# Kernel optimization log

Measured on AMD Instinct MI355X. Metric: run time of the kernel, lower is better.

Reference implementation:

```python
import jax, jax.numpy as jnp
import numpy as np

S, N, F, E, H = 64, 1000, 64, 128, 2  # seq_len, nodes/graph, node_dim, emb_dim, heads
DEG = 8
C = E // H  # per-head channels


def setup_inputs() -> dict:
    key = jax.random.key(0)
    ks = jax.random.split(key, 16)
    Ntot = S * N
    Eg = N * DEG
    src = jax.random.randint(ks[0], (S, Eg), 0, N)
    dst = jax.random.randint(ks[1], (S, Eg), 0, N)
    off = (jnp.arange(S) * N)[:, None]
    edge_index = jnp.stack([(src + off).reshape(-1), (dst + off).reshape(-1)]).astype(jnp.int32)
    nfm = jax.random.normal(ks[2], (Ntot, F), jnp.float32)
    reachable = jax.random.uniform(ks[3], (S, N)) > 0.2
    reachable = reachable.at[:, 0].set(True)  # ensure each row has a reachable node
    h0 = jnp.zeros((N, E), jnp.float32)
    c0 = jnp.zeros((N, E), jnp.float32)

    def lin(k, i, o):
        return (jax.random.normal(k, (i, o), jnp.float32) / np.sqrt(i)).astype(jnp.float32)

    return dict(
        nfm=nfm, edge_index=edge_index, reachable=reachable, h0=h0, c0=c0,
        gat_W1=lin(ks[4], F, E), gat_b1=jnp.zeros((E,), jnp.float32),
        gat_att1=(jax.random.normal(ks[5], (H, C), jnp.float32) / np.sqrt(C)).astype(jnp.float32),
        gat_bias1=jnp.zeros((E,), jnp.float32),
        gat_W=(jax.random.normal(ks[6], (4, E, E), jnp.float32) / np.sqrt(E)).astype(jnp.float32),
        gat_b=jnp.zeros((4, E), jnp.float32),
        gat_att=(jax.random.normal(ks[7], (4, H, C), jnp.float32) / np.sqrt(C)).astype(jnp.float32),
        gat_bias=jnp.zeros((4, E), jnp.float32),
        lstm_Wih=(jax.random.normal(ks[8], (4 * E, E), jnp.float32) / np.sqrt(E)).astype(jnp.float32),
        lstm_Whh=(jax.random.normal(ks[9], (4 * E, E), jnp.float32) / np.sqrt(E)).astype(jnp.float32),
        lstm_bih=jnp.zeros((4 * E,), jnp.float32), lstm_bhh=jnp.zeros((4 * E,), jnp.float32),
        th6_W=lin(ks[10], E, E), th6_b=jnp.zeros((E,), jnp.float32),
        th7_W=lin(ks[11], E, E), th7_b=jnp.zeros((E,), jnp.float32),
        th5_W=lin(ks[12], 2 * E, 1), th5_b=jnp.zeros((1,), jnp.float32),
    )


def _gat_layer(x, src, dst, W, b, att, bias, Ntot):
    # GATv2Conv, share_weights=True: x_l == x_r = lin(x)
    Hh, Ch = att.shape
    xl = (x @ W + b).reshape(-1, Hh, Ch)                 # [Ntot,H,C]
    e = jax.nn.leaky_relu(xl[src] + xl[dst], 0.2)        # [Etot,H,C]
    logit = jnp.einsum('ehc,hc->eh', e, att)             # [Etot,H]
    m = jax.ops.segment_max(logit, dst, num_segments=Ntot)
    a = jnp.exp(logit - m[dst])                          # segment-stable softmax
    denom = jax.ops.segment_sum(a, dst, num_segments=Ntot)
    alpha = a / denom[dst]
    out = jax.ops.segment_sum(xl[src] * alpha[:, :, None], dst, num_segments=Ntot)
    return out.reshape(-1, Hh * Ch) + bias               # concat heads + bias


def _forward(nfm, edge_index, reachable, h0, c0, gat_W1, gat_b1, gat_att1, gat_bias1,
             gat_W, gat_b, gat_att, gat_bias, lstm_Wih, lstm_Whh, lstm_bih, lstm_bhh,
             th6_W, th6_b, th7_W, th7_b, th5_W, th5_b):
    Ntot = nfm.shape[0]
    loops = jnp.arange(Ntot, dtype=edge_index.dtype)     # add_self_loops=True
    src = jnp.concatenate([edge_index[0], loops])
    dst = jnp.concatenate([edge_index[1], loops])

    x = jax.nn.relu(_gat_layer(nfm, src, dst, gat_W1, gat_b1, gat_att1, gat_bias1, Ntot))
    for i in range(4):  # layers 2..5; no activation after last
        x = _gat_layer(x, src, dst, gat_W[i], gat_b[i], gat_att[i], gat_bias[i], Ntot)
        if i < 3:
            x = jax.nn.relu(x)

    mu = x.reshape(S, N, E)                              # [seq, batch(=nodes), emb]

    def step(carry, xt):
        h, c = carry
        g = xt @ lstm_Wih.T + lstm_bih + h @ lstm_Whh.T + lstm_bhh
        i_, f_, gg, o_ = jnp.split(g, 4, axis=-1)        # torch gate order i,f,g,o
        c = jax.nn.sigmoid(f_) * c + jax.nn.sigmoid(i_) * jnp.tanh(gg)
        h = jax.nn.sigmoid(o_) * jnp.tanh(c)
        return (h, c), h

    (hT, cT), mu = jax.lax.scan(step, (h0, c0), mu)      # mu: [S,N,E]

    meanpool = mu.mean(axis=1, keepdims=True)            # [S,1,E]
    gs = meanpool @ th6_W + th6_b
    la = mu @ th7_W + th7_b
    rep = jax.nn.relu(jnp.concatenate([jnp.broadcast_to(gs, la.shape), la], axis=-1))
    logits = (rep @ th5_W)[..., 0] + th5_b               # [S,N]
    logits = jnp.where(reachable, logits, -jnp.inf)
    prob = jax.nn.softmax(logits, axis=1)
    return prob, hT, cT


def reference(nfm, edge_index, reachable, h0, c0, gat_W1, gat_b1, gat_att1, gat_bias1,
              gat_W, gat_b, gat_att, gat_bias, lstm_Wih, lstm_Whh, lstm_bih, lstm_bhh,
              th6_W, th6_b, th7_W, th7_b, th5_W, th5_b):
    return _forward(nfm, edge_index, reachable, h0, c0, gat_W1, gat_b1, gat_att1, gat_bias1,
                    gat_W, gat_b, gat_att, gat_bias, lstm_Wih, lstm_Whh, lstm_bih, lstm_bhh,
                    th6_W, th6_b, th7_W, th7_b, th5_W, th5_b)
```

## Files before the change

kernel.cpp:

```cpp
#include <hip/hip_runtime.h>
#include <hip/hip_bf16.h>

#define SQ   64
#define NN   1000
#define NT   64000
#define EE   128
#define EG   512000
#define ET   576000

#define WS_XA      0ull
#define WS_XB      33000000ull
#define WS_ROWPTR  66000000ull
#define WS_CURSOR  66300000ull
#define WS_SRCS    66600000ull
#define WS_INCL    69000000ull
#define WS_BSUM    69300000ull
#define WS_BOFF    69302048ull
#define WS_MODE    69304096ull
#define WS_WQA     70000000ull
#define WS_WQB     70262144ull
#define WS_AS      70600000ull
#define WS_LOGIT2  70700000ull
#define WS2_XC     33000000ull
#define WS2_BFRAG  164100000ull
#define WS2_GHI    164300000ull
#define WS2_GLO    164650000ull
#define WS2_B512   165000000ull
#define WS2_MODE   165010000ull
#define WS2_AS     165020000ull
#define WS2_LOGIT2 165100000ull
#define WS2_NEED   165360000ull
#define G_W1    0
#define G_WL    8192
#define G_PROJ  73728
#define G_W7    139264

typedef __attribute__((ext_vector_type(8))) short short8;
typedef __attribute__((ext_vector_type(4))) float f32x4;

__device__ __forceinline__ float rdlane(float v, int l) {
    return __int_as_float(__builtin_amdgcn_readlane(__float_as_int(v), l));
}
__device__ __forceinline__ float sigm(float x) { return 1.0f / (1.0f + __expf(-x)); }
__device__ __forceinline__ float tanh_f(float x) {
    x = fminf(fmaxf(x, -30.0f), 30.0f);
    float e = __expf(2.0f * x);
    return (e - 1.0f) / (e + 1.0f);
}
__device__ __forceinline__ float tanh2(float x) {
    return 2.0f / (1.0f + __expf(-2.0f * x)) - 1.0f;
}
__device__ __forceinline__ ushort f2bf(float x) {
    unsigned u = __float_as_uint(x);
    unsigned r = (u + 0x7FFFu + ((u >> 16) & 1u)) >> 16;
    return (ushort)r;
}
__device__ __forceinline__ float bf2f(ushort h) {
    return __uint_as_float(((unsigned)h) << 16);
}

__global__ void detect_mode_k(const unsigned char* __restrict__ p, int* __restrict__ mode) {
    __shared__ int f0, f3;
    const int t = threadIdx.x;
    if (t == 0) { f0 = 0; f3 = 0; }
    __syncthreads();
    int l0 = 0, l3 = 0;
    for (int i = t; i < 16000; i += 256) {
        if (p[4 * i])     l0 = 1;
        if (p[4 * i + 3]) l3 = 1;
    }
    if (l0) atomicOr(&f0, 1);
    if (l3) atomicOr(&f3, 1);
    __syncthreads();
    if (t == 0) {
        int m;
        if (f0 && f3)      m = 1;
        else if (f0)       m = 0;
        else               m = 2;
        *mode = m;
    }
}

__global__ void zero_ints_k(int* __restrict__ p, int n) {
    int i = blockIdx.x * 256 + threadIdx.x;
    if (i < n) p[i] = 0;
}
__global__ void hist_k(const int* __restrict__ ei, int* __restrict__ deg) {
    int e = blockIdx.x * 256 + threadIdx.x;
    if (e < ET) {
        int d = (e < EG) ? ei[EG + e] : (e - EG);
        atomicAdd(deg + d, 1);
    }
}
__global__ void scan1_k(const int* __restrict__ deg, int* __restrict__ incl, int* __restrict__ bsum) {
    __shared__ int sh[256];
    const int t = threadIdx.x;
    const int i = blockIdx.x * 256 + t;
    sh[t] = deg[i];
    __syncthreads();
    for (int o = 1; o < 256; o <<= 1) {
        int add = (t >= o) ? sh[t - o] : 0;
        __syncthreads();
        sh[t] += add;
        __syncthreads();
    }
    incl[i] = sh[t];
    if (t == 255) bsum[blockIdx.x] = sh[255];
}
__global__ void scan2_k(const int* __restrict__ bsum, int* __restrict__ boff) {
    __shared__ int sh[256];
    const int t = threadIdx.x;
    int v = (t < 250) ? bsum[t] : 0;
    sh[t] = v;
    __syncthreads();
    for (int o = 1; o < 256; o <<= 1) {
        int add = (t >= o) ? sh[t - o] : 0;
        __syncthreads();
        sh[t] += add;
        __syncthreads();
    }
    if (t < 250) boff[t] = sh[t] - v;
}
__global__ void scan3_k(const int* __restrict__ incl, const int* __restrict__ boff,
                        int* __restrict__ rowptr, int* __restrict__ cursor_deg) {
    const int i = blockIdx.x * 256 + threadIdx.x;
    int total = incl[i] + boff[blockIdx.x];
    int excl  = total - cursor_deg[i];
    rowptr[i] = excl;
    cursor_deg[i] = excl;
    if (i == NT - 1) rowptr[NT] = total;
}
__global__ void fill_k(const int* __restrict__ ei, int* __restrict__ cursor, int* __restrict__ srcs) {
    int e = blockIdx.x * 256 + threadIdx.x;
    if (e < ET) {
        int s_, d_;
        if (e < EG) { s_ = ei[e]; d_ = ei[EG + e]; }
        else        { s_ = e - EG; d_ = s_; }
        int p = atomicAdd(cursor + d_, 1);
        srcs[p] = s_;
    }
}

__global__ void build_gfrag_k(const float* __restrict__ src, const int ks, const int ns,
                              const int K, ushort* __restrict__ dhi, ushort* __restrict__ dlo,
                              const int total) {
    int id = blockIdx.x * 256 + threadIdx.x;
    if (id < total) {
        int j = id & 7, lane = (id >> 3) & 63;
        int f = id >> 9;
        int KT = K >> 5;
        int nt = f / KT, kt = f - nt * KT;
        int n = nt * 16 + (lane & 15);
        int k = kt * 32 + ((lane >> 4) << 3) + j;
        float v = src[(size_t)k * ks + (size_t)n * ns];
        ushort h = f2bf(v);
        dhi[id] = h;
        dlo[id] = f2bf(v - bf2f(h));
    }
}
__global__ void bias512_k(const float* __restrict__ bih, const float* __restrict__ bhh,
                          float* __restrict__ b512) {
    int i = blockIdx.x * 256 + threadIdx.x;
    if (i < 512) b512[i] = bih[i] + bhh[i];
}

template <int KT>
__global__ __launch_bounds__(256) void gemm_mf(
    const float* __restrict__ x, const ushort* __restrict__ bhi,
    const ushort* __restrict__ blo, const float* __restrict__ bias,
    float* __restrict__ out, const int ldout)
{
    constexpr int K = KT * 32;
    __shared__ __align__(16) ushort ahi_s[64 * 136];
    __shared__ __align__(16) ushort alo_s[64 * 136];
    const int t = threadIdx.x;
    const int w = t >> 6, lane = t & 63;
    const int quad = lane >> 4, col = lane & 15;
    const int row0 = blockIdx.x * 64;
    const int col0 = blockIdx.y * 128;

    {
        const int r  = t >> 2;
        const int kc = (t & 3) * (K / 4);
        const float* xr = x + (size_t)(row0 + r) * K + kc;
        ushort* dh = ahi_s + r * 136 + kc;
        ushort* dl = alo_s + r * 136 + kc;
#pragma unroll
        for (int k = 0; k < K / 4; k += 4) {
            float4 v = *(const float4*)(xr + k);
            ushort h0_ = f2bf(v.x), h1_ = f2bf(v.y), h2_ = f2bf(v.z), h3_ = f2bf(v.w);
            ushort l0_ = f2bf(v.x - bf2f(h0_)), l1_ = f2bf(v.y - bf2f(h1_));
            ushort l2_ = f2bf(v.z - bf2f(h2_)), l3_ = f2bf(v.w - bf2f(h3_));
            *(uint2*)(dh + k) = make_uint2((uint)h0_ | ((uint)h1_ << 16),
                                           (uint)h2_ | ((uint)h3_ << 16));
            *(uint2*)(dl + k) = make_uint2((uint)l0_ | ((uint)l1_ << 16),
                                           (uint)l2_ | ((uint)l3_ << 16));
        }
    }
    __syncthreads();

    short8 ah[KT], al[KT];
#pragma unroll
    for (int kt = 0; kt < KT; kt++) {
        const int off = (w * 16 + col) * 136 + kt * 32 + quad * 8;
        ah[kt] = *(const short8*)(ahi_s + off);
        al[kt] = *(const short8*)(alo_s + off);
    }

    f32x4 acc[8];
#pragma unroll
    for (int q = 0; q < 8; q++) acc[q] = (f32x4){0.f, 0.f, 0.f, 0.f};

#pragma unroll
    for (int q = 0; q < 8; q++) {
#pragma unroll
        for (int kt = 0; kt < KT; kt++) {
            const int f = ((((col0 >> 4) + q) * KT + kt) * 64 + lane) * 8;
            short8 bh = *(const short8*)(bhi + f);
            short8 bl = *(const short8*)(blo + f);
            acc[q] = __builtin_amdgcn_mfma_f32_16x16x32_bf16(ah[kt], bh, acc[q], 0, 0, 0);
            acc[q] = __builtin_amdgcn_mfma_f32_16x16x32_bf16(al[kt], bh, acc[q], 0, 0, 0);
            acc[q] = __builtin_amdgcn_mfma_f32_16x16x32_bf16(ah[kt], bl, acc[q], 0, 0, 0);
        }
    }

#pragma unroll
    for (int q = 0; q < 8; q++) {
        float bv = bias[col0 + q * 16 + col];
#pragma unroll
        for (int r = 0; r < 4; r++) {
            out[(size_t)(row0 + w * 16 + quad * 4 + r) * ldout + col0 + q * 16 + col]
                = acc[q][r] + bv;
        }
    }
}

template <int K>
__global__ __launch_bounds__(256) void gemm3(
    const float* __restrict__ x, const float* __restrict__ W,
    const float* __restrict__ b, float* __restrict__ out)
{
    __shared__ float Wsh[64 * 128];
    __shared__ float xT[64][132];
    const int t = threadIdx.x;
    const int row0 = blockIdx.x * 128;
    const int cg = t & 15;
    const int rg = t >> 4;
    float4 acc[8][2];
#pragma unroll
    for (int r = 0; r < 8; r++) {
        acc[r][0] = make_float4(0.f, 0.f, 0.f, 0.f);
        acc[r][1] = make_float4(0.f, 0.f, 0.f, 0.f);
    }
    for (int k0 = 0; k0 < K; k0 += 64) {
        for (int i = t * 4; i < 64 * 128; i += 1024)
            *(float4*)(Wsh + i) = *(const float4*)(W + (size_t)k0 * 128 + i);
        for (int i = t * 4; i < 128 * 64; i += 1024) {
            int r = i >> 6, k = i & 63;
            float4 v = *(const float4*)(x + (size_t)(row0 + r) * K + k0 + k);
            xT[k + 0][r] = v.x; xT[k + 1][r] = v.y;
            xT[k + 2][r] = v.z; xT[k + 3][r] = v.w;
        }
        __syncthreads();
#pragma unroll 2
        for (int k = 0; k < 64; k++) {
            float4 w0 = *(const float4*)(Wsh + k * 128 + cg * 8);
            float4 w1 = *(const float4*)(Wsh + k * 128 + cg * 8 + 4);
            float4 x0 = *(const float4*)(&xT[k][rg * 8]);
            float4 x1 = *(const float4*)(&xT[k][rg * 8 + 4]);
            float xv[8] = {x0.x, x0.y, x0.z, x0.w, x1.x, x1.y, x1.z, x1.w};
#pragma unroll
            for (int r = 0; r < 8; r++) {
                acc[r][0].x += xv[r] * w0.x; acc[r][0].y += xv[r] * w0.y;
                acc[r][0].z += xv[r] * w0.z; acc[r][0].w += xv[r] * w0.w;
                acc[r][1].x += xv[r] * w1.x; acc[r][1].y += xv[r] * w1.y;
                acc[r][1].z += xv[r] * w1.z; acc[r][1].w += xv[r] * w1.w;
            }
        }
        __syncthreads();
    }
    float4 bv0 = *(const float4*)(b + cg * 8);
    float4 bv1 = *(const float4*)(b + cg * 8 + 4);
#pragma unroll
    for (int r = 0; r < 8; r++) {
        float4 o0, o1;
        o0.x = acc[r][0].x + bv0.x; o0.y = acc[r][0].y + bv0.y;
        o0.z = acc[r][0].z + bv0.z; o0.w = acc[r][0].w + bv0.w;
        o1.x = acc[r][1].x + bv1.x; o1.y = acc[r][1].y + bv1.y;
        o1.z = acc[r][1].z + bv1.z; o1.w = acc[r][1].w + bv1.w;
        float* op = out + (size_t)(row0 + rg * 8 + r) * 128 + cg * 8;
        *(float4*)(op) = o0;
        *(float4*)(op + 4) = o1;
    }
}

__global__ __launch_bounds__(256) void gat_fused_k(
    const float* __restrict__ xl, const int* __restrict__ rowptr,
    const int* __restrict__ srcs, const float* __restrict__ att,
    const float* __restrict__ bias, float* __restrict__ out, const int do_relu)
{
    const int lane = threadIdx.x & 63;
    const int b = blockIdx.x;
    const int g = b & 7;
    const int j = b >> 3;
    const int jq = j / 250;
    const int jj = j - jq * 250;
    const int s = g + 8 * jq;
    const int n = s * NN + jj * 4 + (threadIdx.x >> 6);

    const float2 a = *(const float2*)(att + lane * 2);
    const float2 xd = *(const float2*)(xl + (size_t)n * 128 + lane * 2);
    const int i0 = rowptr[n], i1 = rowptr[n + 1];

    float m0 = -1e30f, d0 = 0.f, ax0 = 0.f, ay0 = 0.f;
    float m1 = -1e30f, d1 = 0.f, ax1 = 0.f, ay1 = 0.f;

    int i = i0;
    int sv0 = srcs[i];
    int sv1 = (i + 1 < i1) ? srcs[i + 1] : 0;
    while (i + 1 < i1) {
        const float2 xs0 = *(const float2*)(xl + (size_t)sv0 * 128 + lane * 2);
        const float2 xs1 = *(const float2*)(xl + (size_t)sv1 * 128 + lane * 2);
        sv0 = (i + 2 < i1) ? srcs[i + 2] : 0;
        sv1 = (i + 3 < i1) ? srcs[i + 3] : 0;

        float u0 = xs0.x + xd.x, v0 = xs0.y + xd.y;
        float u1 = xs1.x + xd.x, v1 = xs1.y + xd.y;
        u0 = (u0 > 0.f) ? u0 : 0.2f * u0;  v0 = (v0 > 0.f) ? v0 : 0.2f * v0;
        u1 = (u1 > 0.f) ? u1 : 0.2f * u1;  v1 = (v1 > 0.f) ? v1 : 0.2f * v1;
        float p0 = u0 * a.x + v0 * a.y;
        float p1 = u1 * a.x + v1 * a.y;
        p0 += __shfl_xor(p0, 1, 32);   p1 += __shfl_xor(p1, 1, 32);
        p0 += __shfl_xor(p0, 2, 32);   p1 += __shfl_xor(p1, 2, 32);
        p0 += __shfl_xor(p0, 4, 32);   p1 += __shfl_xor(p1, 4, 32);
        p0 += __shfl_xor(p0, 8, 32);   p1 += __shfl_xor(p1, 8, 32);
        p0 += __shfl_xor(p0, 16, 32);  p1 += __shfl_xor(p1, 16, 32);

        float mn0 = fmaxf(m0, p0),  mn1 = fmaxf(m1, p1);
        float sc0 = __expf(m0 - mn0), sc1 = __expf(m1 - mn1);
        float w0 = __expf(p0 - mn0),  w1 = __expf(p1 - mn1);
        d0 = d0 * sc0 + w0;             d1 = d1 * sc1 + w1;
        ax0 = ax0 * sc0 + w0 * xs0.x;   ax1 = ax1 * sc1 + w1 * xs1.x;
        ay0 = ay0 * sc0 + w0 * xs0.y;   ay1 = ay1 * sc1 + w1 * xs1.y;
        m0 = mn0;                       m1 = mn1;
        i += 2;
    }
    if (i < i1) {
        const float2 xs0 = *(const float2*)(xl + (size_t)sv0 * 128 + lane * 2);
        float u0 = xs0.x + xd.x, v0 = xs0.y + xd.y;
        u0 = (u0 > 0.f) ? u0 : 0.2f * u0;  v0 = (v0 > 0.f) ? v0 : 0.2f * v0;
        float p0 = u0 * a.x + v0 * a.y;
        p0 += __shfl_xor(p0, 1, 32);
        p0 += __shfl_xor(p0, 2, 32);
        p0 += __shfl_xor(p0, 4, 32);
        p0 += __shfl_xor(p0, 8, 32);
        p0 += __shfl_xor(p0, 16, 32);
        float mn0 = fmaxf(m0, p0);
        float sc0 = __expf(m0 - mn0), w0 = __expf(p0 - mn0);
        d0 = d0 * sc0 + w0;
        ax0 = ax0 * sc0 + w0 * xs0.x;
        ay0 = ay0 * sc0 + w0 * xs0.y;
        m0 = mn0;
    }
    float mm = fmaxf(m0, m1);
    float s0 = __expf(m0 - mm), s1 = __expf(m1 - mm);
    float den = d0 * s0 + d1 * s1;
    float ax = ax0 * s0 + ax1 * s1;
    float ay = ay0 * s0 + ay1 * s1;

    float2 bv = *(const float2*)(bias + lane * 2);
    float inv = 1.f / den;
    float ox = ax * inv + bv.x, oy = ay * inv + bv.y;
    if (do_relu) { ox = fmaxf(ox, 0.f); oy = fmaxf(oy, 0.f); }
    *(float2*)(out + (size_t)n * 128 + lane * 2) = make_float2(ox, oy);
}

__global__ void build_wq_k(const float* __restrict__ Wih, const float* __restrict__ Whh,
                           float4* __restrict__ WQa, float4* __restrict__ WQb) {
    int id = blockIdx.x * 256 + threadIdx.x;
    if (id < 64 * 256) {
        int kp = id >> 8, t = id & 255;
        int j1 = t, j2 = t + 256;
        WQa[id] = make_float4(Wih[(size_t)j1 * 128 + 2 * kp], Whh[(size_t)j1 * 128 + 2 * kp],
                              Wih[(size_t)j1 * 128 + 2 * kp + 1], Whh[(size_t)j1 * 128 + 2 * kp + 1]);
        WQb[id] = make_float4(Wih[(size_t)j2 * 128 + 2 * kp], Whh[(size_t)j2 * 128 + 2 * kp],
                              Wih[(size_t)j2 * 128 + 2 * kp + 1], Whh[(size_t)j2 * 128 + 2 * kp + 1]);
    }
}

__global__ void build_bfrag_k(const float* __restrict__ Whh, ushort* __restrict__ Bfrag) {
    int id = blockIdx.x * 256 + threadIdx.x;
    if (id < 65536) {
        int j = id & 7, lane = (id >> 3) & 63, kt = (id >> 9) & 3, tile = id >> 11;
        int gate = tile * 16 + (lane & 15);
        int k = kt * 32 + ((lane >> 4) << 3) + j;
        Bfrag[id] = f2bf(Whh[(size_t)gate * 128 + k]);
    }
}

#define LSTM_GROUP(buf, gbase)                                                     \
    _Pragma("unroll")                                                              \
    for (int i_ = 0; i_ < 4; i_++) {                                               \
        const int kp_ = (gbase) * 4 + i_;                                          \
        const float4 qa_ = buf[i_];                                                \
        const float4 qb_ = buf[4 + i_];                                            \
        _Pragma("unroll")                                                          \
        for (int n_ = 0; n_ < 4; n_++) {                                           \
            const float sx0_ = rdlane(xr[n_].x, kp_);                              \
            const float sh0_ = rdlane(hr[n_].x, kp_);                              \
            const float sx1_ = rdlane(xr[n_].y, kp_);                              \
            const float sh1_ = rdlane(hr[n_].y, kp_);                              \
            acc1[n_] += sx0_ * qa_.x + sh0_ * qa_.y + sx1_ * qa_.z + sh1_ * qa_.w; \
            acc2[n_] += sx0_ * qb_.x + sh0_ * qb_.y + sx1_ * qb_.z + sh1_ * qb_.w; \
        }                                                                          \
    }

__global__ __launch_bounds__(256, 1) void lstm_k(
    float* __restrict__ mu, const float4* __restrict__ WQa, const float4* __restrict__ WQb,
    const float* __restrict__ bih, const float* __restrict__ bhh,
    const float* __restrict__ h0, const float* __restrict__ c0,
    float* __restrict__ hT, float* __restrict__ cT)
{
    const int t = threadIdx.x, lane = t & 63;
    const int n0 = blockIdx.x * 4;
    __shared__ float hsh[4][128];
    __shared__ float gsh[4][512];
    const float b1 = bih[t] + bhh[t];
    const float b2 = bih[t + 256] + bhh[t + 256];
    float creg[2];
#pragma unroll
    for (int q = 0; q < 2; q++) {
        int id = t + 256 * q;
        creg[q] = c0[(size_t)(n0 + (id >> 7)) * 128 + (id & 127)];
    }
    for (int i = t; i < 512; i += 256)
        hsh[i >> 7][i & 127] = h0[(size_t)(n0 + (i >> 7)) * 128 + (i & 127)];

    const float4* pA = WQa + t;
    const float4* pB = WQb + t;

    float2 xr[4], xnx[4];
#pragma unroll
    for (int n = 0; n < 4; n++)
        xr[n] = *(const float2*)(mu + (size_t)n0 * 128 + n * 128 + lane * 2);
    __syncthreads();

    for (int s = 0; s < SQ; s++) {
        float* xrow = mu + ((size_t)s * NN + n0) * 128;
        float2 hr[4];
#pragma unroll
        for (int n = 0; n < 4; n++) hr[n] = *(const float2*)(&hsh[n][lane * 2]);

        float4 bufA[8], bufB[8];
#pragma unroll
        for (int i = 0; i < 4; i++) { bufA[i] = pA[i * 256]; bufA[4 + i] = pB[i * 256]; }

        if (s + 1 < SQ) {
            const float* xrow2 = mu + ((size_t)(s + 1) * NN + n0) * 128;
#pragma unroll
            for (int n = 0; n < 4; n++) xnx[n] = *(const float2*)(xrow2 + n * 128 + lane * 2);
        }

        float acc1[4], acc2[4];
#pragma unroll
        for (int n = 0; n < 4; n++) { acc1[n] = b1; acc2[n] = b2; }

        for (int g = 0; g < 16; g += 2) {
#pragma unroll
            for (int i = 0; i < 4; i++) {
                bufB[i]     = pA[((g + 1) * 4 + i) * 256];
                bufB[4 + i] = pB[((g + 1) * 4 + i) * 256];
            }
            LSTM_GROUP(bufA, g)
            if (g < 14) {
#pragma unroll
                for (int i = 0; i < 4; i++) {
                    bufA[i]     = pA[((g + 2) * 4 + i) * 256];
                    bufA[4 + i] = pB[((g + 2) * 4 + i) * 256];
                }
            }
            LSTM_GROUP(bufB, g + 1)
        }

#pragma unroll
        for (int n = 0; n < 4; n++) { gsh[n][t] = acc1[n]; gsh[n][t + 256] = acc2[n]; }
        __syncthreads();
#pragma unroll
        for (int q = 0; q < 2; q++) {
            int id = t + 256 * q;
            int n = id >> 7, e = id & 127;
            float iv = gsh[n][e], fv = gsh[n][128 + e];
            float gv = gsh[n][256 + e], ov = gsh[n][384 + e];
            float c = sigm(fv) * creg[q] + sigm(iv) * tanh_f(gv);
            float h = sigm(ov) * tanh_f(c);
            creg[q] = c;
            hsh[n][e] = h;
            xrow[n * 128 + e] = h;
            if (s == SQ - 1) {
                hT[(size_t)(n0 + n) * 128 + e] = h;
                cT[(size_t)(n0 + n) * 128 + e] = c;
            }
        }
#pragma unroll
        for (int n = 0; n < 4; n++) xr[n] = xnx[n];
        __syncthreads();
    }
}

__global__ __launch_bounds__(512, 2) void lstm8_k(
    float* __restrict__ mu, const float* __restrict__ xC,
    const ushort* __restrict__ Bfrag,
    const float* __restrict__ h0, const float* __restrict__ c0,
    float* __restrict__ hT, float* __restrict__ cT)
{
    const int t = threadIdx.x;
    const int w = t >> 6, lane = t & 63;
    const int quad = lane >> 4, col = lane & 15;
    const int n0 = blockIdx.x * 4;
    const int enode = t >> 7;
    const int ech   = t & 127;

    __shared__ __align__(16) ushort hbuf[2][2][16 * 136];
    __shared__ float gsh[4][512];

    short8 bf[4][4];
#pragma unroll
    for (int g4 = 0; g4 < 4; g4++)
#pragma unroll
        for (int kt = 0; kt < 4; kt++) {
            int tile = g4 * 8 + w;
            bf[g4][kt] = *(const short8*)(Bfrag + (((tile * 4 + kt) * 64 + lane) << 3));
        }

    for (int i = t; i < 2048; i += 512) {
        int node = i >> 7, ee = i & 127;
        float v = (node < 4) ? h0[(size_t)(n0 + node) * 128 + ee] : 0.f;
        ushort hh = f2bf(v), hl = f2bf(v - bf2f(hh));
        hbuf[0][0][node * 136 + ee] = hh; hbuf[0][1][node * 136 + ee] = hl;
        hbuf[1][0][node * 136 + ee] = hh; hbuf[1][1][node * 136 + ee] = hl;
    }
    float cst = c0[(size_t)(n0 + enode) * 128 + ech];

    float xcr[4], xcn[4];
#pragma unroll
    for (int g4 = 0; g4 < 4; g4++)
        xcr[g4] = xC[((size_t)(n0 + enode)) * 512 + g4 * 128 + ech];
    __syncthreads();

    int p = 0;
    for (int s = 0; s < SQ; s++) {
        if (s + 1 < SQ) {
            const float* xn = xC + ((size_t)(s + 1) * NN + n0 + enode) * 512;
#pragma unroll
            for (int g4 = 0; g4 < 4; g4++)
                xcn[g4] = xn[g4 * 128 + ech];
        }

        short8 ahi[4], alo[4];
#pragma unroll
        for (int kt = 0; kt < 4; kt++) {
            ahi[kt] = *(const short8*)(&hbuf[p][0][col * 136 + kt * 32 + quad * 8]);
            alo[kt] = *(const short8*)(&hbuf[p][1][col * 136 + kt * 32 + quad * 8]);
        }

        f32x4 acc[4];
#pragma unroll
        for (int g4 = 0; g4 < 4; g4++) acc[g4] = (f32x4){0.f, 0.f, 0.f, 0.f};
#pragma unroll
        for (int kt = 0; kt < 4; kt++) {
#pragma unroll
            for (int g4 = 0; g4 < 4; g4++)
                acc[g4] = __builtin_amdgcn_mfma_f32_16x16x32_bf16(ahi[kt], bf[g4][kt], acc[g4], 0, 0, 0);
#pragma unroll
            for (int g4 = 0; g4 < 4; g4++)
                acc[g4] = __builtin_amdgcn_mfma_f32_16x16x32_bf16(alo[kt], bf[g4][kt], acc[g4], 0, 0, 0);
        }

        if (quad == 0) {
#pragma unroll
            for (int g4 = 0; g4 < 4; g4++)
#pragma unroll
                for (int r = 0; r < 4; r++)
                    gsh[r][(g4 * 8 + w) * 16 + col] = acc[g4][r];
        }
        __syncthreads();

        {
            float iv = gsh[enode][0 * 128 + ech] + xcr[0];
            float fv = gsh[enode][1 * 128 + ech] + xcr[1];
            float gv = gsh[enode][2 * 128 + ech] + xcr[2];
            float ov = gsh[enode][3 * 128 + ech] + xcr[3];
            float c = sigm(fv) * cst + sigm(iv) * tanh2(gv);
            float h = sigm(ov) * tanh2(c);
            cst = c;
            const int pn = p ^ 1;
            ushort hh = f2bf(h);
            hbuf[pn][0][enode * 136 + ech] = hh;
            hbuf[pn][1][enode * 136 + ech] = f2bf(h - bf2f(hh));
            mu[((size_t)s * NN + n0 + enode) * 128 + ech] = h;
            if (s == SQ - 1) {
                hT[(size_t)(n0 + enode) * 128 + ech] = h;
                cT[(size_t)(n0 + enode) * 128 + ech] = c;
            }
            p = pn;
        }
#pragma unroll
        for (int g4 = 0; g4 < 4; g4++) xcr[g4] = xcn[g4];
        __syncthreads();
    }
}

__global__ __launch_bounds__(256) void meanpool_gs_k(
    const float* __restrict__ mu, const float* __restrict__ W6,
    const float* __restrict__ b6, const float* __restrict__ w5,
    float* __restrict__ A)
{
    const int s = blockIdx.x, t = threadIdx.x;
    const int ch = t & 127, half = t >> 7;
    __shared__ float mp[128];
    __shared__ float red[256];
    float acc = 0.f;
    for (int n = half * 500; n < (half + 1) * 500; n++)
        acc += mu[((size_t)s * NN + n) * 128 + ch];
    red[t] = acc;
    __syncthreads();
    if (t < 128) mp[t] = (red[t] + red[t + 128]) * 0.001f;
    __syncthreads();
    float g = 0.f;
    if (t < 128) {
        g = b6[t];
        for (int k = 0; k < 128; k++) g += mp[k] * W6[(size_t)k * 128 + t];
        g = fmaxf(g, 0.f) * w5[t];
    }
    red[t] = g;
    __syncthreads();
    for (int o = 128; o > 0; o >>= 1) {
        if (t < o) red[t] += red[t + o];
        __syncthreads();
    }
    if (t == 0) A[s] = red[0];
}

__global__ __launch_bounds__(256) void rowdot_k(
    const float* __restrict__ la, const float* __restrict__ w5,
    const float* __restrict__ b5, const float* __restrict__ A,
    float* __restrict__ out)
{
    const int lane = threadIdx.x & 63;
    const int row = blockIdx.x * 4 + (threadIdx.x >> 6);
    float2 v = *(const float2*)(la + (size_t)row * 128 + lane * 2);
    float2 w = *(const float2*)(w5 + 128 + lane * 2);
    float x = fmaxf(v.x, 0.f) * w.x + fmaxf(v.y, 0.f) * w.y;
#pragma unroll
    for (int o = 32; o; o >>= 1) x += __shfl_down(x, o);
    if (lane == 0) out[row] = x + A[row / NN] + b5[0];
}

__device__ __forceinline__ bool reach_at(const void* reach, int mode, int idx) {
    if (mode == 0) return ((const int*)reach)[idx] != 0;
    if (mode == 1) return ((const unsigned char*)reach)[idx] != 0;
    return ((const float*)reach)[idx] != 0.f;
}
__global__ __launch_bounds__(256) void softmax_k(
    const float* __restrict__ lg, const void* __restrict__ reach,
    const int* __restrict__ mode, float* __restrict__ prob)
{
    const int s = blockIdx.x, t = threadIdx.x;
    const int m = *mode;
    __shared__ float red[256];
    float mx = -1e30f;
    for (int i = t; i < NN; i += 256) {
        int idx = s * NN + i;
        if (reach_at(reach, m, idx)) mx = fmaxf(mx, lg[idx]);
    }
    red[t] = mx;
    __syncthreads();
    for (int o = 128; o; o >>= 1) {
        if (t < o) red[t] = fmaxf(red[t], red[t + o]);
        __syncthreads();
    }
    mx = red[0];
    __syncthreads();
    float sum = 0.f;
    for (int i = t; i < NN; i += 256) {
        int idx = s * NN + i;
        float v = reach_at(reach, m, idx) ? __expf(lg[idx] - mx) : 0.f;
        prob[idx] = v;
        sum += v;
    }
    red[t] = sum;
    __syncthreads();
    for (int o = 128; o; o >>= 1) {
        if (t < o) red[t] += red[t + o];
        __syncthreads();
    }
    float inv = 1.f / red[0];
    for (int i = t; i < NN; i += 256) prob[s * NN + i] *= inv;
}

extern "C" void kernel_launch(void* const* d_in, const int* in_sizes, int n_in,
                              void* d_out, int out_size, void* d_ws, size_t ws_size,
                              hipStream_t stream) {
    const float* nfm   = (const float*)d_in[0];
    const int*   ei    = (const int*)d_in[1];
    const void*  reach = d_in[2];
    const float* h0    = (const float*)d_in[3];
    const float* c0    = (const float*)d_in[4];
    const float* W1    = (const float*)d_in[5];
    const float* b1    = (const float*)d_in[6];
    const float* att1  = (const float*)d_in[7];
    const float* bias1 = (const float*)d_in[8];
    const float* Wl    = (const float*)d_in[9];
    const float* bl    = (const float*)d_in[10];
    const float* attl  = (const float*)d_in[11];
    const float* biasl = (const float*)d_in[12];
    const float* Wih   = (const float*)d_in[13];
    const float* Whh   = (const float*)d_in[14];
    const float* bih   = (const float*)d_in[15];
    const float* bhh   = (const float*)d_in[16];
    const float* W6    = (const float*)d_in[17];
    const float* b6    = (const float*)d_in[18];
    const float* W7    = (const float*)d_in[19];
    const float* b7    = (const float*)d_in[20];
    const float* w5    = (const float*)d_in[21];
    const float* b5    = (const float*)d_in[22];

    char* ws = (char*)d_ws;
    const bool bigws = (ws_size >= WS2_NEED);

    float*  xA     = (float*)(ws + WS_XA);
    float*  xB     = (float*)(ws + WS_XB);
    int*    rowptr = (int*)(ws + WS_ROWPTR);
    int*    cursor = (int*)(ws + WS_CURSOR);
    int*    srcs   = (int*)(ws + WS_SRCS);
    int*    incl   = (int*)(ws + WS_INCL);
    int*    bsum   = (int*)(ws + WS_BSUM);
    int*    boff   = (int*)(ws + WS_BOFF);
    int*    modep  = bigws ? (int*)(ws + WS2_MODE)     : (int*)(ws + WS_MODE);
    float*  As     = bigws ? (float*)(ws + WS2_AS)     : (float*)(ws + WS_AS);
    float*  logit2 = bigws ? (float*)(ws + WS2_LOGIT2) : (float*)(ws + WS_LOGIT2);
    float*  xC     = (float*)(ws + WS2_XC);
    ushort* Bfrag  = (ushort*)(ws + WS2_BFRAG);
    ushort* ghi    = (ushort*)(ws + WS2_GHI);
    ushort* glo    = (ushort*)(ws + WS2_GLO);
    float*  b512   = (float*)(ws + WS2_B512);
    float4* WQa    = (float4*)(ws + WS_WQA);
    float4* WQb    = (float4*)(ws + WS_WQB);

    float* prob = (float*)d_out;
    float* hT   = (float*)d_out + 64000;
    float* cT   = (float*)d_out + 192000;

    detect_mode_k<<<1, 256, 0, stream>>>((const unsigned char*)reach, modep);
    zero_ints_k<<<250, 256, 0, stream>>>(cursor, NT);
    hist_k<<<2250, 256, 0, stream>>>(ei, cursor);
    scan1_k<<<250, 256, 0, stream>>>(cursor, incl, bsum);
    scan2_k<<<1, 256, 0, stream>>>(bsum, boff);
    scan3_k<<<250, 256, 0, stream>>>(incl, boff, rowptr, cursor);
    fill_k<<<2250, 256, 0, stream>>>(ei, cursor, srcs);
    if (bigws) {
        build_bfrag_k<<<256, 256, 0, stream>>>(Whh, Bfrag);
        bias512_k<<<2, 256, 0, stream>>>(bih, bhh, b512);
        build_gfrag_k<<<32, 256, 0, stream>>>(W1, 128, 1, 64, ghi + G_W1, glo + G_W1, 8192);
        for (int i = 0; i < 4; i++)
            build_gfrag_k<<<64, 256, 0, stream>>>(Wl + (size_t)i * 16384, 128, 1, 128,
                                                  ghi + G_WL + i * 16384, glo + G_WL + i * 16384, 16384);
        build_gfrag_k<<<256, 256, 0, stream>>>(Wih, 1, 128, 128, ghi + G_PROJ, glo + G_PROJ, 65536);
        build_gfrag_k<<<64, 256, 0, stream>>>(W7, 128, 1, 128, ghi + G_W7, glo + G_W7, 16384);
    } else {
        build_wq_k<<<64, 256, 0, stream>>>(Wih, Whh, WQa, WQb);
    }

    for (int l = 0; l < 5; l++) {
        if (bigws) {
            if (l == 0)
                gemm_mf<2><<<dim3(1000, 1), 256, 0, stream>>>(nfm, ghi + G_W1, glo + G_W1, b1, xB, 128);
            else
                gemm_mf<4><<<dim3(1000, 1), 256, 0, stream>>>(xA, ghi + G_WL + (l - 1) * 16384,
                                                              glo + G_WL + (l - 1) * 16384,
                                                              bl + (l - 1) * 128, xB, 128);
        } else {
            if (l == 0)
                gemm3<64><<<500, 256, 0, stream>>>(nfm, W1, b1, xB);
            else
                gemm3<128><<<500, 256, 0, stream>>>(xA, Wl + (size_t)(l - 1) * 128 * 128,
                                                    bl + (l - 1) * 128, xB);
        }
        const float* att  = (l == 0) ? att1  : attl  + (l - 1) * 128;
        const float* bias = (l == 0) ? bias1 : biasl + (l - 1) * 128;
        gat_fused_k<<<16000, 256, 0, stream>>>(xB, rowptr, srcs, att, bias, xA,
                                               (l < 4) ? 1 : 0);
    }

    if (bigws) {
        gemm_mf<4><<<dim3(1000, 4), 256, 0, stream>>>(xA, ghi + G_PROJ, glo + G_PROJ, b512, xC, 512);
        lstm8_k<<<250, 512, 0, stream>>>(xA, xC, Bfrag, h0, c0, hT, cT);
    } else {
        lstm_k<<<250, 256, 0, stream>>>(xA, WQa, WQb, bih, bhh, h0, c0, hT, cT);
    }

    meanpool_gs_k<<<64, 256, 0, stream>>>(xA, W6, b6, w5, As);
    if (bigws)
        gemm_mf<4><<<dim3(1000, 1), 256, 0, stream>>>(xA, ghi + G_W7, glo + G_W7, b7, xB, 128);
    else
        gemm3<128><<<500, 256, 0, stream>>>(xA, W7, b7, xB);
    rowdot_k<<<16000, 256, 0, stream>>>(xB, w5, b5, As, logit2);
    softmax_k<<<64, 256, 0, stream>>>(logit2, reach, modep, prob);
}
```

Before: 739.9 us.

## Split GAT edges across half-waves and halve nodes per LSTM block

The GAT aggregation kernel now has each half of a 64-lane wavefront handle alternate edges using float4 channel loads. The two partial online-softmax states are merged with cross-half shuffles, which removes the serial two-stream loop and its tail handling. The LSTM recurrence kernel now processes 2 nodes per block instead of 4 and launches 500 blocks, so more CUs run the latency-bound sequential scan. The cost is that half of the MFMA rows and half of the epilogue threads sit idle in each block.

```diff
diff --git a/kernel.cpp b/kernel.cpp
--- a/kernel.cpp
+++ b/kernel.cpp
@@ -300,6 +300,8 @@
     const float* __restrict__ bias, float* __restrict__ out, const int do_relu)
 {
     const int lane = threadIdx.x & 63;
+    const int q = lane & 31;
+    const int h = lane >> 5;
     const int b = blockIdx.x;
     const int g = b & 7;
     const int j = b >> 3;
@@ -308,71 +310,61 @@
     const int s = g + 8 * jq;
     const int n = s * NN + jj * 4 + (threadIdx.x >> 6);
 
-    const float2 a = *(const float2*)(att + lane * 2);
-    const float2 xd = *(const float2*)(xl + (size_t)n * 128 + lane * 2);
+    const float4 a4 = *(const float4*)(att + q * 4);
+    const float4 xd = *(const float4*)(xl + (size_t)n * 128 + q * 4);
     const int i0 = rowptr[n], i1 = rowptr[n + 1];
 
-    float m0 = -1e30f, d0 = 0.f, ax0 = 0.f, ay0 = 0.f;
-    float m1 = -1e30f, d1 = 0.f, ax1 = 0.f, ay1 = 0.f;
-
-    int i = i0;
-    int sv0 = srcs[i];
-    int sv1 = (i + 1 < i1) ? srcs[i + 1] : 0;
-    while (i + 1 < i1) {
-        const float2 xs0 = *(const float2*)(xl + (size_t)sv0 * 128 + lane * 2);
-        const float2 xs1 = *(const float2*)(xl + (size_t)sv1 * 128 + lane * 2);
-        sv0 = (i + 2 < i1) ? srcs[i + 2] : 0;
-        sv1 = (i + 3 < i1) ? srcs[i + 3] : 0;
-
-        float u0 = xs0.x + xd.x, v0 = xs0.y + xd.y;
-        float u1 = xs1.x + xd.x, v1 = xs1.y + xd.y;
-        u0 = (u0 > 0.f) ? u0 : 0.2f * u0;  v0 = (v0 > 0.f) ? v0 : 0.2f * v0;
-        u1 = (u1 > 0.f) ? u1 : 0.2f * u1;  v1 = (v1 > 0.f) ? v1 : 0.2f * v1;
-        float p0 = u0 * a.x + v0 * a.y;
-        float p1 = u1 * a.x + v1 * a.y;
-        p0 += __shfl_xor(p0, 1, 32);   p1 += __shfl_xor(p1, 1, 32);
-        p0 += __shfl_xor(p0, 2, 32);   p1 += __shfl_xor(p1, 2, 32);
-        p0 += __shfl_xor(p0, 4, 32);   p1 += __shfl_xor(p1, 4, 32);
-        p0 += __shfl_xor(p0, 8, 32);   p1 += __shfl_xor(p1, 8, 32);
-        p0 += __shfl_xor(p0, 16, 32);  p1 += __shfl_xor(p1, 16, 32);
-
-        float mn0 = fmaxf(m0, p0),  mn1 = fmaxf(m1, p1);
-        float sc0 = __expf(m0 - mn0), sc1 = __expf(m1 - mn1);
-        float w0 = __expf(p0 - mn0),  w1 = __expf(p1 - mn1);
-        d0 = d0 * sc0 + w0;             d1 = d1 * sc1 + w1;
-        ax0 = ax0 * sc0 + w0 * xs0.x;   ax1 = ax1 * sc1 + w1 * xs1.x;
-        ay0 = ay0 * sc0 + w0 * xs0.y;   ay1 = ay1 * sc1 + w1 * xs1.y;
-        m0 = mn0;                       m1 = mn1;
-        i += 2;
-    }
-    if (i < i1) {
-        const float2 xs0 = *(const float2*)(xl + (size_t)sv0 * 128 + lane * 2);
-        float u0 = xs0.x + xd.x, v0 = xs0.y + xd.y;
-        u0 = (u0 > 0.f) ? u0 : 0.2f * u0;  v0 = (v0 > 0.f) ? v0 : 0.2f * v0;
-        float p0 = u0 * a.x + v0 * a.y;
-        p0 += __shfl_xor(p0, 1, 32);
-        p0 += __shfl_xor(p0, 2, 32);
-        p0 += __shfl_xor(p0, 4, 32);
-        p0 += __shfl_xor(p0, 8, 32);
-        p0 += __shfl_xor(p0, 16, 32);
-        float mn0 = fmaxf(m0, p0);
-        float sc0 = __expf(m0 - mn0), w0 = __expf(p0 - mn0);
-        d0 = d0 * sc0 + w0;
-        ax0 = ax0 * sc0 + w0 * xs0.x;
-        ay0 = ay0 * sc0 + w0 * xs0.y;
-        m0 = mn0;
-    }
-    float mm = fmaxf(m0, m1);
-    float s0 = __expf(m0 - mm), s1 = __expf(m1 - mm);
-    float den = d0 * s0 + d1 * s1;
-    float ax = ax0 * s0 + ax1 * s1;
-    float ay = ay0 * s0 + ay1 * s1;
-
-    float2 bv = *(const float2*)(bias + lane * 2);
+    float m = -1e30f, d = 0.f;
+    float ax = 0.f, ay = 0.f, az = 0.f, aw = 0.f;
+
+    for (int base = i0, i = i0 + h; base < i1; base += 2, i += 2) {
+        const bool valid = (i < i1);
+        int sv = 0;
+        if (valid) sv = srcs[i];
+        const float4 xs = *(const float4*)(xl + (size_t)sv * 128 + q * 4);
+        float u0 = xs.x + xd.x, u1 = xs.y + xd.y;
+        float u2 = xs.z + xd.z, u3 = xs.w + xd.w;
+        float p;
+        p  = a4.x * fmaxf(u0, 0.2f * u0);
+        p += a4.y * fmaxf(u1, 0.2f * u1);
+        p += a4.z * fmaxf(u2, 0.2f * u2);
+        p += a4.w * fmaxf(u3, 0.2f * u3);
+        p += __shfl_xor(p, 1);
+        p += __shfl_xor(p, 2);
+        p += __shfl_xor(p, 4);
+        p += __shfl_xor(p, 8);
+        float mn = fmaxf(m, valid ? p : -1e30f);
+        float sc = __expf(m - mn);
+        float wgt = valid ? __expf(p - mn) : 0.f;
+        d  = d  * sc + wgt;
+        ax = ax * sc + wgt * xs.x;
+        ay = ay * sc + wgt * xs.y;
+        az = az * sc + wgt * xs.z;
+        aw = aw * sc + wgt * xs.w;
+        m = mn;
+    }
+
+    float m2 = __shfl_xor(m, 32);
+    float d2 = __shfl_xor(d, 32);
+    float bx = __shfl_xor(ax, 32);
+    float by = __shfl_xor(ay, 32);
+    float bz = __shfl_xor(az, 32);
+    float bw = __shfl_xor(aw, 32);
+    float mm = fmaxf(m, m2);
+    float s1 = __expf(m - mm), s2 = __expf(m2 - mm);
+    float den = d * s1 + d2 * s2;
     float inv = 1.f / den;
-    float ox = ax * inv + bv.x, oy = ay * inv + bv.y;
-    if (do_relu) { ox = fmaxf(ox, 0.f); oy = fmaxf(oy, 0.f); }
-    *(float2*)(out + (size_t)n * 128 + lane * 2) = make_float2(ox, oy);
+    float4 bv = *(const float4*)(bias + q * 4);
+    float ox = (ax * s1 + bx * s2) * inv + bv.x;
+    float oy = (ay * s1 + by * s2) * inv + bv.y;
+    float oz = (az * s1 + bz * s2) * inv + bv.z;
+    float ow = (aw * s1 + bw * s2) * inv + bv.w;
+    if (do_relu) {
+        ox = fmaxf(ox, 0.f); oy = fmaxf(oy, 0.f);
+        oz = fmaxf(oz, 0.f); ow = fmaxf(ow, 0.f);
+    }
+    if (lane < 32)
+        *(float4*)(out + (size_t)n * 128 + q * 4) = make_float4(ox, oy, oz, ow);
 }
 
 __global__ void build_wq_k(const float* __restrict__ Wih, const float* __restrict__ Whh,
@@ -507,7 +499,7 @@
     }
 }
 
-__global__ __launch_bounds__(512, 2) void lstm8_k(
+__global__ __launch_bounds__(512, 2) void lstm9_k(
     float* __restrict__ mu, const float* __restrict__ xC,
     const ushort* __restrict__ Bfrag,
     const float* __restrict__ h0, const float* __restrict__ c0,
@@ -516,12 +508,13 @@
     const int t = threadIdx.x;
     const int w = t >> 6, lane = t & 63;
     const int quad = lane >> 4, col = lane & 15;
-    const int n0 = blockIdx.x * 4;
-    const int enode = t >> 7;
+    const int n0 = blockIdx.x * 2;
+    const int enode = (t >> 7) & 1;
     const int ech   = t & 127;
+    const bool epi  = (t < 256);
 
     __shared__ __align__(16) ushort hbuf[2][2][16 * 136];
-    __shared__ float gsh[4][512];
+    __shared__ float gsh[2][512];
 
     short8 bf[4][4];
 #pragma unroll
@@ -534,22 +527,24 @@
 
     for (int i = t; i < 2048; i += 512) {
         int node = i >> 7, ee = i & 127;
-        float v = (node < 4) ? h0[(size_t)(n0 + node) * 128 + ee] : 0.f;
+        float v = (node < 2) ? h0[(size_t)(n0 + node) * 128 + ee] : 0.f;
         ushort hh = f2bf(v), hl = f2bf(v - bf2f(hh));
         hbuf[0][0][node * 136 + ee] = hh; hbuf[0][1][node * 136 + ee] = hl;
         hbuf[1][0][node * 136 + ee] = hh; hbuf[1][1][node * 136 + ee] = hl;
     }
-    float cst = c0[(size_t)(n0 + enode) * 128 + ech];
-
+    float cst = 0.f;
     float xcr[4], xcn[4];
-#pragma unroll
-    for (int g4 = 0; g4 < 4; g4++)
-        xcr[g4] = xC[((size_t)(n0 + enode)) * 512 + g4 * 128 + ech];
+    if (epi) {
+        cst = c0[(size_t)(n0 + enode) * 128 + ech];
+#pragma unroll
+        for (int g4 = 0; g4 < 4; g4++)
+            xcr[g4] = xC[((size_t)(n0 + enode)) * 512 + g4 * 128 + ech];
+    }
     __syncthreads();
 
     int p = 0;
     for (int s = 0; s < SQ; s++) {
-        if (s + 1 < SQ) {
+        if (epi && s + 1 < SQ) {
             const float* xn = xC + ((size_t)(s + 1) * NN + n0 + enode) * 512;
 #pragma unroll
             for (int g4 = 0; g4 < 4; g4++)
@@ -580,12 +575,12 @@
 #pragma unroll
             for (int g4 = 0; g4 < 4; g4++)
 #pragma unroll
-                for (int r = 0; r < 4; r++)
+                for (int r = 0; r < 2; r++)
                     gsh[r][(g4 * 8 + w) * 16 + col] = acc[g4][r];
         }
         __syncthreads();
 
-        {
+        if (epi) {
             float iv = gsh[enode][0 * 128 + ech] + xcr[0];
             float fv = gsh[enode][1 * 128 + ech] + xcr[1];
             float gv = gsh[enode][2 * 128 + ech] + xcr[2];
@@ -602,10 +597,10 @@
                 hT[(size_t)(n0 + enode) * 128 + ech] = h;
                 cT[(size_t)(n0 + enode) * 128 + ech] = c;
             }
-            p = pn;
-        }
-#pragma unroll
-        for (int g4 = 0; g4 < 4; g4++) xcr[g4] = xcn[g4];
+#pragma unroll
+            for (int g4 = 0; g4 < 4; g4++) xcr[g4] = xcn[g4];
+        }
+        p ^= 1;
         __syncthreads();
     }
 }
@@ -794,7 +789,7 @@
 
     if (bigws) {
         gemm_mf<4><<<dim3(1000, 4), 256, 0, stream>>>(xA, ghi + G_PROJ, glo + G_PROJ, b512, xC, 512);
-        lstm8_k<<<250, 512, 0, stream>>>(xA, xC, Bfrag, h0, c0, hT, cT);
+        lstm9_k<<<500, 512, 0, stream>>>(xA, xC, Bfrag, h0, c0, hT, cT);
     } else {
         lstm_k<<<250, 256, 0, stream>>>(xA, WQa, WQb, bih, bhh, h0, c0, hT, cT);
     }
```

After: 732.5 us. About the same (-1.0%).
